# Performance work log

Measured on AMD Instinct MI355X. Metric: run time of the kernel, lower is better.

## Reference

```python
import jax, jax.numpy as jnp
import numpy as np

NUM_HEADS = 16
NUM_LANDMARKS = 64
N_ITER = 6


def iterative_inv(mat):
    # mat: (B, H, L, L) row-stochastic kernel; Newton-Schulz-style iteration
    L = mat.shape[-1]
    I = jnp.eye(L, dtype=mat.dtype)
    K = mat
    # init: V = K^T / max_j(sum_i K_ij)
    denom = jnp.max(jnp.sum(K, axis=-2), axis=-1)[:, :, None, None]
    Vm = (1.0 / denom) * jnp.swapaxes(K, -1, -2)
    for _ in range(N_ITER):
        KV = jnp.matmul(K, Vm)
        Vm = jnp.matmul(0.25 * Vm, 13.0 * I - jnp.matmul(KV, 15.0 * I - jnp.matmul(KV, 7.0 * I - KV)))
    return Vm


def setup_inputs() -> dict:
    key = jax.random.key(0)
    kq, kk, kv = jax.random.split(key, 3)
    B, N, C = 4, 4096, 1024
    return {
        "Q": jax.random.normal(kq, (B, N, C), dtype=jnp.float32),
        "K": jax.random.normal(kk, (B, N, C), dtype=jnp.float32),
        "V": jax.random.normal(kv, (B, N, C), dtype=jnp.float32),
    }


def reference(Q, K, V):
    B, N, C = Q.shape
    H, Lm = NUM_HEADS, NUM_LANDMARKS
    hd = C // H
    scale = hd ** 0.5
    # (B, H, N, hd)
    q = Q.reshape(B, N, H, hd).transpose(0, 2, 1, 3) / scale
    k = K.reshape(B, N, H, hd).transpose(0, 2, 1, 3)
    v = V.reshape(B, N, H, hd).transpose(0, 2, 1, 3)

    # landmark pooling (N divisible by Lm): mean over segments of length N//Lm
    seg = N // Lm
    k_lm = k.reshape(B, H, Lm, seg, hd).mean(axis=-2)  # (B,H,Lm,hd)
    q_lm = q.reshape(B, H, Lm, seg, hd).mean(axis=-2)  # (B,H,Lm,hd)

    kernel_1 = jax.nn.softmax(jnp.einsum('bhnd,bhld->bhnl', q, k_lm), axis=-1)   # (B,H,N,Lm)
    kernel_2 = jax.nn.softmax(jnp.einsum('bhmd,bhld->bhml', q_lm, k_lm), axis=-1)  # (B,H,Lm,Lm)
    kernel_3 = jax.nn.softmax(jnp.einsum('bhld,bhnd->bhln', q_lm, k), axis=-1)   # (B,H,Lm,N)

    out = jnp.matmul(jnp.matmul(kernel_1, iterative_inv(kernel_2)), jnp.matmul(kernel_3, v))
    return out.transpose(0, 2, 1, 3).reshape(B, N, C)
```

## Files before the change

kernel.cpp:

```cpp
#include <hip/hip_runtime.h>
#include <math.h>

#define BB 4
#define NN 4096
#define CC 1024
#define HH 16
#define HD 64
#define LM 64
#define SEG 64
#define BHN (BB*HH)
#define MATP 68
#define MATE (64*MATP)
#define KS 68

typedef __attribute__((ext_vector_type(8))) short bf16x8;
typedef __attribute__((ext_vector_type(4))) short s16x4;
typedef __attribute__((ext_vector_type(4))) float f32x4;

__device__ __forceinline__ float shfl_sum16(float v) {
  v += __shfl_xor(v, 1, 16);
  v += __shfl_xor(v, 2, 16);
  v += __shfl_xor(v, 4, 16);
  v += __shfl_xor(v, 8, 16);
  return v;
}

__device__ __forceinline__ void split8(const float* f, bf16x8& hi, bf16x8& lo) {
#pragma unroll
  for (int i = 0; i < 8; ++i) {
    unsigned u = __builtin_bit_cast(unsigned, f[i]);
    float hf = __builtin_bit_cast(float, u & 0xFFFF0000u);
    hi[i] = (short)(u >> 16);
    float l = f[i] - hf;
    unsigned ul = __builtin_bit_cast(unsigned, l);
    lo[i] = (short)(ul >> 16);
  }
}

__device__ __forceinline__ void split4(const float* f, s16x4& hi, s16x4& lo) {
#pragma unroll
  for (int i = 0; i < 4; ++i) {
    unsigned u = __builtin_bit_cast(unsigned, f[i]);
    float hf = __builtin_bit_cast(float, u & 0xFFFF0000u);
    hi[i] = (short)(u >> 16);
    float l = f[i] - hf;
    unsigned ul = __builtin_bit_cast(unsigned, l);
    lo[i] = (short)(ul >> 16);
  }
}

__device__ __forceinline__ bf16x8 ld8(const short* __restrict__ P, int row, int kb) {
  s16x4 a = *(const s16x4*)&P[row*KS + kb];
  s16x4 b = *(const s16x4*)&P[row*KS + kb + 4];
  bf16x8 r;
  r[0]=a[0]; r[1]=a[1]; r[2]=a[2]; r[3]=a[3];
  r[4]=b[0]; r[5]=b[1]; r[6]=b[2]; r[7]=b[3];
  return r;
}

__device__ __forceinline__ bf16x8 ldT8(const short* __restrict__ P, int row, int kb, int sw) {
  const char* base = (const char*)P + row*136;
  s16x4 a = *(const s16x4*)(base + ((2*kb) ^ sw));
  s16x4 b = *(const s16x4*)(base + ((2*kb + 8) ^ sw));
  bf16x8 r;
  r[0]=a[0]; r[1]=a[1]; r[2]=a[2]; r[3]=a[3];
  r[4]=b[0]; r[5]=b[1]; r[6]=b[2]; r[7]=b[3];
  return r;
}

__device__ __forceinline__ void xpose4(float x[4], int lane) {
  bool p1 = (lane >> 4) & 1;
  float s0 = p1 ? x[0] : x[1], s1 = p1 ? x[2] : x[3];
  float r0 = __shfl_xor(s0, 16, 64), r1 = __shfl_xor(s1, 16, 64);
  if (p1) { x[0] = r0; x[2] = r1; } else { x[1] = r0; x[3] = r1; }
  bool p2 = (lane >> 5) & 1;
  s0 = p2 ? x[0] : x[2]; s1 = p2 ? x[1] : x[3];
  r0 = __shfl_xor(s0, 32, 64); r1 = __shfl_xor(s1, 32, 64);
  if (p2) { x[0] = r0; x[1] = r1; } else { x[2] = r0; x[3] = r1; }
}

__global__ __launch_bounds__(256) void lm_kernel(
    const float* __restrict__ Q, const float* __restrict__ K,
    float* __restrict__ qlm, float* __restrict__ klm) {
  int bh = blockIdx.y; int b = bh >> 4; int h = bh & 15;
  int tid = threadIdx.x;
  int l = blockIdx.x * 4 + (tid >> 6);
  int d = tid & 63;
  const float* qbase = Q + ((size_t)b*NN + (size_t)l*SEG)*CC + h*HD + d;
  const float* kbase = K + ((size_t)b*NN + (size_t)l*SEG)*CC + h*HD + d;
  float sq = 0.f, sk = 0.f;
#pragma unroll 8
  for (int s = 0; s < SEG; ++s) {
    sq += qbase[(size_t)s*CC];
    sk += kbase[(size_t)s*CC];
  }
  qlm[(size_t)bh*4096 + l*64 + d] = sq * (1.0f/(64.0f*8.0f));
  klm[(size_t)bh*4096 + l*64 + d] = sk * (1.0f/64.0f);
}

__global__ __launch_bounds__(256, 3) void k3v_kernel(
    const float* __restrict__ K, const float* __restrict__ V,
    const float* __restrict__ qlm,
    float* __restrict__ S3, float* __restrict__ ACC3) {
  __shared__ short KEh[64*KS], KEl[64*KS];
  __shared__ short VtH[64*KS], VtL[64*KS];
  __shared__ float Erow[64*MATP];
  const int bh = blockIdx.y, b = bh >> 4, h = bh & 15;
  const int tile = blockIdx.x, tid = threadIdx.x;
  const int wid = tid >> 6, lane = tid & 63;
  const int lr = lane & 15, lg = lane >> 4;
  const int m0 = wid*16 + lg*4;

  bf16x8 qh[2], ql[2];
#pragma unroll
  for (int ks = 0; ks < 2; ++ks) {
    const float* qp = qlm + (size_t)bh*4096 + (wid*16 + lr)*64 + ks*32 + lg*8;
    float qf[8];
    *(float4*)&qf[0] = *(const float4*)qp;
    *(float4*)&qf[4] = *(const float4*)(qp + 4);
    split8(qf, qh[ks], ql[ks]);
  }

  f32x4 acc2[4];
#pragma unroll
  for (int t = 0; t < 4; ++t) acc2[t] = (f32x4){0.f, 0.f, 0.f, 0.f};
  float srow[4] = {0.f, 0.f, 0.f, 0.f};

  for (int sub = 0; sub < 4; ++sub) {
    const int n0 = tile*256 + sub*64;
    __syncthreads();
#pragma unroll
    for (int q = 0; q < 4; ++q) {
      int f = tid + 256*q;
      int r = f >> 4, c4 = (f & 15) << 2;
      size_t g = ((size_t)b*NN + n0 + r)*CC + h*HD + c4;
      float4 kv = *(const float4*)&K[g];
      s16x4 kh, kl; split4((const float*)&kv, kh, kl);
      *(s16x4*)&KEh[r*KS + c4] = kh;
      *(s16x4*)&KEl[r*KS + c4] = kl;
      float4 vv = *(const float4*)&V[g];
      float x[4] = {vv.x, vv.y, vv.z, vv.w};
      xpose4(x, lane);
      int d = 4*(lane & 15) + (lane >> 4);
      int nb = 16*q + 4*wid;
      s16x4 vh, vl; split4(x, vh, vl);
      char* pv = (char*)VtH + d*136 + ((2*nb) ^ ((d & 15) << 3));
      char* pl = (char*)VtL + d*136 + ((2*nb) ^ ((d & 15) << 3));
      *(s16x4*)pv = vh;
      *(s16x4*)pl = vl;
    }
    __syncthreads();

    f32x4 zacc[4];
#pragma unroll
    for (int t = 0; t < 4; ++t) zacc[t] = (f32x4){0.f, 0.f, 0.f, 0.f};
#pragma unroll
    for (int ks = 0; ks < 2; ++ks) {
      const int kb = ks*32 + lg*8;
#pragma unroll
      for (int tn = 0; tn < 4; ++tn) {
        bf16x8 bh_ = ld8(KEh, tn*16 + lr, kb);
        bf16x8 bl_ = ld8(KEl, tn*16 + lr, kb);
        zacc[tn] = __builtin_amdgcn_mfma_f32_16x16x32_bf16(qh[ks], bh_, zacc[tn], 0, 0, 0);
        zacc[tn] = __builtin_amdgcn_mfma_f32_16x16x32_bf16(qh[ks], bl_, zacc[tn], 0, 0, 0);
        zacc[tn] = __builtin_amdgcn_mfma_f32_16x16x32_bf16(ql[ks], bh_, zacc[tn], 0, 0, 0);
      }
    }
    float e[4][4];
#pragma unroll
    for (int tn = 0; tn < 4; ++tn)
#pragma unroll
      for (int r = 0; r < 4; ++r) e[tn][r] = expf(zacc[tn][r]);
#pragma unroll
    for (int r = 0; r < 4; ++r) {
      float t = e[0][r] + e[1][r] + e[2][r] + e[3][r];
      srow[r] += shfl_sum16(t);
    }
#pragma unroll
    for (int tn = 0; tn < 4; ++tn) {
      const int n = tn*16 + lr;
#pragma unroll
      for (int r = 0; r < 4; ++r) Erow[(m0 + r)*MATP + n] = e[tn][r];
    }

#pragma unroll
    for (int ks = 0; ks < 2; ++ks) {
      const int kb = ks*32 + lg*8;
      float fa[8];
      const float* ap = Erow + (wid*16 + lr)*MATP + kb;
      *(float4*)&fa[0] = *(const float4*)ap;
      *(float4*)&fa[4] = *(const float4*)(ap + 4);
      bf16x8 ah, al; split8(fa, ah, al);
      const int sw = lr << 3;
#pragma unroll
      for (int tn = 0; tn < 4; ++tn) {
        bf16x8 bh_ = ldT8(VtH, tn*16 + lr, kb, sw);
        bf16x8 bl_ = ldT8(VtL, tn*16 + lr, kb, sw);
        acc2[tn] = __builtin_amdgcn_mfma_f32_16x16x32_bf16(ah, bh_, acc2[tn], 0, 0, 0);
        acc2[tn] = __builtin_amdgcn_mfma_f32_16x16x32_bf16(ah, bl_, acc2[tn], 0, 0, 0);
        acc2[tn] = __builtin_amdgcn_mfma_f32_16x16x32_bf16(al, bh_, acc2[tn], 0, 0, 0);
      }
    }
  }

  if (lr == 0) {
#pragma unroll
    for (int r = 0; r < 4; ++r)
      atomicAdd(&S3[bh*64 + m0 + r], srow[r]);
  }
#pragma unroll
  for (int tn = 0; tn < 4; ++tn)
#pragma unroll
    for (int r = 0; r < 4; ++r)
      atomicAdd(&ACC3[(size_t)bh*4096 + (m0 + r)*64 + tn*16 + lr], acc2[tn][r]);
}

template<bool FUSE, bool HR, bool HC, bool HG>
__device__ __forceinline__ void mm_mfma(
    const float* __restrict__ Arow, const float* __restrict__ Scol,
    float diagc, float scale,
    float* __restrict__ OutRow, float* __restrict__ OutCol, float* __restrict__ OutGlob,
    int wid, int lane) {
  const int lr = lane & 15, lg = lane >> 4;
  f32x4 acc[4];
#pragma unroll
  for (int t = 0; t < 4; ++t) acc[t] = (f32x4){0.f, 0.f, 0.f, 0.f};

#pragma unroll
  for (int ks = 0; ks < 2; ++ks) {
    const int kb = ks*32 + lg*8;
    float fa[8];
    const float* ap = Arow + (wid*16 + lr)*MATP + kb;
#pragma unroll
    for (int i = 0; i < 4; ++i) { float2 t = *(const float2*)(ap + 2*i); fa[2*i] = t.x; fa[2*i+1] = t.y; }
    bf16x8 ah, al; split8(fa, ah, al);
#pragma unroll
    for (int tn = 0; tn < 4; ++tn) {
      float fb[8];
      const float* bp = Scol + (tn*16 + lr)*MATP + kb;
#pragma unroll
      for (int i = 0; i < 4; ++i) { float2 t = *(const float2*)(bp + 2*i); fb[2*i] = t.x; fb[2*i+1] = t.y; }
      if (FUSE) {
        int diff = (tn*16 + lr) - kb;
#pragma unroll
        for (int i = 0; i < 8; ++i) fb[i] = (i == diff ? diagc : 0.f) - fb[i];
      }
      bf16x8 bh_, bl_; split8(fb, bh_, bl_);
      acc[tn] = __builtin_amdgcn_mfma_f32_16x16x32_bf16(ah, bh_, acc[tn], 0, 0, 0);
      acc[tn] = __builtin_amdgcn_mfma_f32_16x16x32_bf16(ah, bl_, acc[tn], 0, 0, 0);
      acc[tn] = __builtin_amdgcn_mfma_f32_16x16x32_bf16(al, bh_, acc[tn], 0, 0, 0);
    }
  }
  __syncthreads();
#pragma unroll
  for (int tn = 0; tn < 4; ++tn) {
    float v0 = scale*acc[tn][0], v1 = scale*acc[tn][1], v2 = scale*acc[tn][2], v3 = scale*acc[tn][3];
    const int n = tn*16 + lr, m0 = wid*16 + lg*4;
    if (HC) *(float4*)&OutCol[n*MATP + m0] = make_float4(v0, v1, v2, v3);
    if (HR) {
      OutRow[(m0+0)*MATP + n] = v0;
      OutRow[(m0+1)*MATP + n] = v1;
      OutRow[(m0+2)*MATP + n] = v2;
      OutRow[(m0+3)*MATP + n] = v3;
    }
    if (HG) {
      OutGlob[(m0+0)*64 + n] = v0;
      OutGlob[(m0+1)*64 + n] = v1;
      OutGlob[(m0+2)*64 + n] = v2;
      OutGlob[(m0+3)*64 + n] = v3;
    }
  }
  __syncthreads();
}

__global__ __launch_bounds__(256) void inv_kernel(
    const float* __restrict__ qlm, const float* __restrict__ klm,
    const float* __restrict__ S3, const float* __restrict__ ACC3,
    float* __restrict__ W) {
  extern __shared__ float sm[];
  float* K2row = sm;
  float* Vmrow = sm + 1*MATE;
  float* Vmcol = sm + 2*MATE;
  float* Xrow  = sm + 3*MATE;
  float* Xcol  = sm + 4*MATE;
  float* Ycol  = sm + 5*MATE;
  float* Zcol  = sm + 6*MATE;
  float* red   = sm + 7*MATE;
  const int bh = blockIdx.x, tid = threadIdx.x;
  const int wid = tid >> 6, lane = tid & 63;
  const int lr = lane & 15, lg = lane >> 4;

#pragma unroll
  for (int q = 0; q < 4; ++q) {
    int f = tid + 256*q;
    int r = f >> 4, c4 = (f & 15) << 2;
    *(float4*)&Xrow[r*MATP + c4] = *(const float4*)&qlm[(size_t)bh*4096 + f*4];
    *(float4*)&Xcol[r*MATP + c4] = *(const float4*)&klm[(size_t)bh*4096 + f*4];
  }
  __syncthreads();

  {
    f32x4 zacc[4];
#pragma unroll
    for (int t = 0; t < 4; ++t) zacc[t] = (f32x4){0.f, 0.f, 0.f, 0.f};
#pragma unroll
    for (int ks = 0; ks < 2; ++ks) {
      const int kb = ks*32 + lg*8;
      float fa[8];
      const float* ap = Xrow + (wid*16 + lr)*MATP + kb;
#pragma unroll
      for (int i = 0; i < 4; ++i) { float2 t = *(const float2*)(ap + 2*i); fa[2*i] = t.x; fa[2*i+1] = t.y; }
      bf16x8 ah, al; split8(fa, ah, al);
#pragma unroll
      for (int tn = 0; tn < 4; ++tn) {
        float fb[8];
        const float* bp = Xcol + (tn*16 + lr)*MATP + kb;
#pragma unroll
        for (int i = 0; i < 4; ++i) { float2 t = *(const float2*)(bp + 2*i); fb[2*i] = t.x; fb[2*i+1] = t.y; }
        bf16x8 bh_, bl_; split8(fb, bh_, bl_);
        zacc[tn] = __builtin_amdgcn_mfma_f32_16x16x32_bf16(ah, bh_, zacc[tn], 0, 0, 0);
        zacc[tn] = __builtin_amdgcn_mfma_f32_16x16x32_bf16(ah, bl_, zacc[tn], 0, 0, 0);
        zacc[tn] = __builtin_amdgcn_mfma_f32_16x16x32_bf16(al, bh_, zacc[tn], 0, 0, 0);
      }
    }
    __syncthreads();
    float e[4][4];
#pragma unroll
    for (int tn = 0; tn < 4; ++tn)
#pragma unroll
      for (int r = 0; r < 4; ++r) e[tn][r] = expf(zacc[tn][r]);
#pragma unroll
    for (int r = 0; r < 4; ++r) {
      float t = e[0][r] + e[1][r] + e[2][r] + e[3][r];
      t = shfl_sum16(t);
      float ri = 1.0f / t;
#pragma unroll
      for (int tn = 0; tn < 4; ++tn) e[tn][r] *= ri;
    }
    const int m0 = wid*16 + lg*4;
#pragma unroll
    for (int tn = 0; tn < 4; ++tn) {
      const int n = tn*16 + lr;
#pragma unroll
      for (int r = 0; r < 4; ++r) K2row[(m0+r)*MATP + n] = e[tn][r];
    }
  }
  __syncthreads();

  if (tid < 64) {
    float c = 0.f;
#pragma unroll 8
    for (int i = 0; i < 64; ++i) c += K2row[i*MATP + tid];
#pragma unroll
    for (int m = 1; m < 64; m <<= 1) c = fmaxf(c, __shfl_xor(c, m, 64));
    if (tid == 0) red[0] = 1.0f / c;
  }
  __syncthreads();
  const float invden = red[0];

#pragma unroll
  for (int q = 0; q < 4; ++q) {
    int f = tid + 256*q;
    int i = f >> 4, c4 = (f & 15) << 2;
    float4 kv = *(const float4*)&K2row[i*MATP + c4];
    kv.x *= invden; kv.y *= invden; kv.z *= invden; kv.w *= invden;
    *(float4*)&Vmcol[i*MATP + c4] = kv;
    Vmrow[(c4+0)*MATP + i] = kv.x;
    Vmrow[(c4+1)*MATP + i] = kv.y;
    Vmrow[(c4+2)*MATP + i] = kv.z;
    Vmrow[(c4+3)*MATP + i] = kv.w;
  }
  __syncthreads();

  for (int it = 0; it < 6; ++it) {
    mm_mfma<false, true,  true,  false>(K2row, Vmcol, 0.f,  1.0f,  Xrow, Xcol, nullptr, wid, lane);
    mm_mfma<true,  false, true,  false>(Xrow,  Xcol,  7.f,  1.0f,  nullptr, Ycol, nullptr, wid, lane);
    mm_mfma<true,  false, true,  false>(Xrow,  Ycol,  15.f, 1.0f,  nullptr, Zcol, nullptr, wid, lane);
    mm_mfma<true,  true,  true,  false>(Vmrow, Zcol,  13.f, 0.25f, Vmrow, Vmcol, nullptr, wid, lane);
  }

#pragma unroll
  for (int q = 0; q < 4; ++q) {
    int f = tid + 256*q;
    int k = f >> 4, c4 = (f & 15) << 2;
    float4 tv = *(const float4*)&ACC3[(size_t)bh*4096 + f*4];
    float ri = 1.0f / S3[bh*64 + k];
    Ycol[(c4+0)*MATP + k] = tv.x * ri;
    Ycol[(c4+1)*MATP + k] = tv.y * ri;
    Ycol[(c4+2)*MATP + k] = tv.z * ri;
    Ycol[(c4+3)*MATP + k] = tv.w * ri;
  }
  __syncthreads();
  mm_mfma<false, false, false, true>(Vmrow, Ycol, 0.f, 1.0f, nullptr, nullptr, W + (size_t)bh*4096, wid, lane);
}

__global__ __launch_bounds__(256, 3) void out_kernel(
    const float* __restrict__ Q, const float* __restrict__ klm,
    const float* __restrict__ W, float* __restrict__ Out) {
  __shared__ short KlH[64*KS], KlL[64*KS];
  __shared__ short WtH[64*KS], WtL[64*KS];
  __shared__ float Prow[64*MATP];
  const int bh = blockIdx.y, b = bh >> 4, h = bh & 15;
  const int n0 = blockIdx.x * 64;
  const int tid = threadIdx.x;
  const int wid = tid >> 6, lane = tid & 63;
  const int lr = lane & 15, lg = lane >> 4;
  const int m0 = wid*16 + lg*4;

#pragma unroll
  for (int q = 0; q < 4; ++q) {
    int f = tid + 256*q;
    int r = f >> 4, c4 = (f & 15) << 2;
    float4 kl = *(const float4*)&klm[(size_t)bh*4096 + f*4];
    s16x4 kh, kll; split4((const float*)&kl, kh, kll);
    *(s16x4*)&KlH[r*KS + c4] = kh;
    *(s16x4*)&KlL[r*KS + c4] = kll;
    float4 wv = *(const float4*)&W[(size_t)bh*4096 + f*4];
    float x[4] = {wv.x, wv.y, wv.z, wv.w};
    xpose4(x, lane);
    int d = 4*(lane & 15) + (lane >> 4);
    int nb = 16*q + 4*wid;
    s16x4 wh, wl; split4(x, wh, wl);
    char* pv = (char*)WtH + d*136 + ((2*nb) ^ ((d & 15) << 3));
    char* pl = (char*)WtL + d*136 + ((2*nb) ^ ((d & 15) << 3));
    *(s16x4*)pv = wh;
    *(s16x4*)pl = wl;
  }

  bf16x8 qh[2], ql[2];
#pragma unroll
  for (int ks = 0; ks < 2; ++ks) {
    const float* qp = Q + ((size_t)b*NN + n0 + wid*16 + lr)*CC + h*HD + ks*32 + lg*8;
    float qf[8];
    *(float4*)&qf[0] = *(const float4*)qp;
    *(float4*)&qf[4] = *(const float4*)(qp + 4);
#pragma unroll
    for (int i = 0; i < 8; ++i) qf[i] *= 0.125f;
    split8(qf, qh[ks], ql[ks]);
  }
  __syncthreads();

  f32x4 zacc[4];
#pragma unroll
  for (int t = 0; t < 4; ++t) zacc[t] = (f32x4){0.f, 0.f, 0.f, 0.f};
#pragma unroll
  for (int ks = 0; ks < 2; ++ks) {
    const int kb = ks*32 + lg*8;
#pragma unroll
    for (int tn = 0; tn < 4; ++tn) {
      bf16x8 bh_ = ld8(KlH, tn*16 + lr, kb);
      bf16x8 bl_ = ld8(KlL, tn*16 + lr, kb);
      zacc[tn] = __builtin_amdgcn_mfma_f32_16x16x32_bf16(qh[ks], bh_, zacc[tn], 0, 0, 0);
      zacc[tn] = __builtin_amdgcn_mfma_f32_16x16x32_bf16(qh[ks], bl_, zacc[tn], 0, 0, 0);
      zacc[tn] = __builtin_amdgcn_mfma_f32_16x16x32_bf16(ql[ks], bh_, zacc[tn], 0, 0, 0);
    }
  }
  float e[4][4];
#pragma unroll
  for (int tn = 0; tn < 4; ++tn)
#pragma unroll
    for (int r = 0; r < 4; ++r) e[tn][r] = expf(zacc[tn][r]);
#pragma unroll
  for (int r = 0; r < 4; ++r) {
    float t = e[0][r] + e[1][r] + e[2][r] + e[3][r];
    t = shfl_sum16(t);
    float ri = 1.0f / t;
#pragma unroll
    for (int tn = 0; tn < 4; ++tn) e[tn][r] *= ri;
  }
#pragma unroll
  for (int tn = 0; tn < 4; ++tn) {
    const int n = tn*16 + lr;
#pragma unroll
    for (int r = 0; r < 4; ++r) Prow[(m0+r)*MATP + n] = e[tn][r];
  }

  f32x4 oacc[4];
#pragma unroll
  for (int t = 0; t < 4; ++t) oacc[t] = (f32x4){0.f, 0.f, 0.f, 0.f};
#pragma unroll
  for (int ks = 0; ks < 2; ++ks) {
    const int kb = ks*32 + lg*8;
    float fa[8];
    const float* ap = Prow + (wid*16 + lr)*MATP + kb;
    *(float4*)&fa[0] = *(const float4*)ap;
    *(float4*)&fa[4] = *(const float4*)(ap + 4);
    bf16x8 ah, al; split8(fa, ah, al);
    const int sw = lr << 3;
#pragma unroll
    for (int tn = 0; tn < 4; ++tn) {
      bf16x8 bh_ = ldT8(WtH, tn*16 + lr, kb, sw);
      bf16x8 bl_ = ldT8(WtL, tn*16 + lr, kb, sw);
      oacc[tn] = __builtin_amdgcn_mfma_f32_16x16x32_bf16(ah, bh_, oacc[tn], 0, 0, 0);
      oacc[tn] = __builtin_amdgcn_mfma_f32_16x16x32_bf16(ah, bl_, oacc[tn], 0, 0, 0);
      oacc[tn] = __builtin_amdgcn_mfma_f32_16x16x32_bf16(al, bh_, oacc[tn], 0, 0, 0);
    }
  }
#pragma unroll
  for (int tn = 0; tn < 4; ++tn) {
    const int d = tn*16 + lr;
#pragma unroll
    for (int r = 0; r < 4; ++r)
      Out[((size_t)b*NN + n0 + m0 + r)*CC + h*HD + d] = oacc[tn][r];
  }
}

extern "C" void kernel_launch(void* const* d_in, const int* in_sizes, int n_in,
                              void* d_out, int out_size, void* d_ws, size_t ws_size,
                              hipStream_t stream) {
  const float* Q = (const float*)d_in[0];
  const float* K = (const float*)d_in[1];
  const float* V = (const float*)d_in[2];
  float* out = (float*)d_out;
  float* ws  = (float*)d_ws;

  float* qlm  = ws;
  float* klm  = ws + 262144;
  float* S3   = ws + 524288;
  float* ACC3 = ws + 528384;
  float* Wm   = ws + 790528;

  size_t shC = (size_t)(7*MATE + 4)*sizeof(float);
  hipFuncSetAttribute((const void*)inv_kernel,
                      hipFuncAttributeMaxDynamicSharedMemorySize, (int)shC);

  hipMemsetAsync(S3, 0, (4096 + 262144)*sizeof(float), stream);

  lm_kernel <<<dim3(16, BHN), 256, 0, stream>>>(Q, K, qlm, klm);
  k3v_kernel<<<dim3(16, BHN), 256, 0, stream>>>(K, V, qlm, S3, ACC3);
  inv_kernel<<<dim3(BHN),     256, shC, stream>>>(qlm, klm, S3, ACC3, Wm);
  out_kernel<<<dim3(64, BHN), 256, 0, stream>>>(Q, klm, Wm, out);
}
```

Measured before the change: 171.7 us.

## Swizzle LDS into dense 128-bit planes, prefetch K/V tiles, double k3v grid

Switches the bf16 hi/lo LDS tiles to an unpadded 128-byte-row layout with an XOR swizzle, so B-operand fragments load as single 128-bit reads instead of two 64-bit reads. The k3v kernel now handles 128 rows per block on a grid twice as large, and loads the next tile's K/V from global memory into registers while computing the current tile. expf is replaced by __expf in the softmax paths. The changes add register pressure and more atomic adds into the shared accumulators, and slightly reduce exp accuracy.

```diff
diff --git a/kernel.cpp b/kernel.cpp
--- a/kernel.cpp
+++ b/kernel.cpp
@@ -11,7 +11,6 @@
 #define BHN (BB*HH)
 #define MATP 68
 #define MATE (64*MATP)
-#define KS 68
 
 typedef __attribute__((ext_vector_type(8))) short bf16x8;
 typedef __attribute__((ext_vector_type(4))) short s16x4;
@@ -49,23 +48,12 @@
   }
 }
 
-__device__ __forceinline__ bf16x8 ld8(const short* __restrict__ P, int row, int kb) {
-  s16x4 a = *(const s16x4*)&P[row*KS + kb];
-  s16x4 b = *(const s16x4*)&P[row*KS + kb + 4];
-  bf16x8 r;
-  r[0]=a[0]; r[1]=a[1]; r[2]=a[2]; r[3]=a[3];
-  r[4]=b[0]; r[5]=b[1]; r[6]=b[2]; r[7]=b[3];
-  return r;
-}
-
-__device__ __forceinline__ bf16x8 ldT8(const short* __restrict__ P, int row, int kb, int sw) {
-  const char* base = (const char*)P + row*136;
-  s16x4 a = *(const s16x4*)(base + ((2*kb) ^ sw));
-  s16x4 b = *(const s16x4*)(base + ((2*kb + 8) ^ sw));
-  bf16x8 r;
-  r[0]=a[0]; r[1]=a[1]; r[2]=a[2]; r[3]=a[3];
-  r[4]=b[0]; r[5]=b[1]; r[6]=b[2]; r[7]=b[3];
-  return r;
+__device__ __forceinline__ int planeAddr(int row, int cd) {
+  int B = (row << 7) + (cd << 4);
+  return B ^ ((row & 7) << 4);
+}
+__device__ __forceinline__ bf16x8 ldP(const short* __restrict__ P, int row, int cd) {
+  return *(const bf16x8*)((const char*)P + planeAddr(row, cd));
 }
 
 __device__ __forceinline__ void xpose4(float x[4], int lane) {
@@ -102,9 +90,9 @@
     const float* __restrict__ K, const float* __restrict__ V,
     const float* __restrict__ qlm,
     float* __restrict__ S3, float* __restrict__ ACC3) {
-  __shared__ short KEh[64*KS], KEl[64*KS];
-  __shared__ short VtH[64*KS], VtL[64*KS];
-  __shared__ float Erow[64*MATP];
+  __shared__ alignas(16) short KEh[64*64], KEl[64*64];
+  __shared__ alignas(16) short VtH[64*64], VtL[64*64];
+  __shared__ alignas(16) float Erow[64*MATP];
   const int bh = blockIdx.y, b = bh >> 4, h = bh & 15;
   const int tile = blockIdx.x, tid = threadIdx.x;
   const int wid = tid >> 6, lane = tid & 63;
@@ -126,82 +114,112 @@
   for (int t = 0; t < 4; ++t) acc2[t] = (f32x4){0.f, 0.f, 0.f, 0.f};
   float srow[4] = {0.f, 0.f, 0.f, 0.f};
 
-  for (int sub = 0; sub < 4; ++sub) {
-    const int n0 = tile*256 + sub*64;
-    __syncthreads();
-#pragma unroll
-    for (int q = 0; q < 4; ++q) {
-      int f = tid + 256*q;
-      int r = f >> 4, c4 = (f & 15) << 2;
-      size_t g = ((size_t)b*NN + n0 + r)*CC + h*HD + c4;
-      float4 kv = *(const float4*)&K[g];
-      s16x4 kh, kl; split4((const float*)&kv, kh, kl);
-      *(s16x4*)&KEh[r*KS + c4] = kh;
-      *(s16x4*)&KEl[r*KS + c4] = kl;
-      float4 vv = *(const float4*)&V[g];
-      float x[4] = {vv.x, vv.y, vv.z, vv.w};
-      xpose4(x, lane);
-      int d = 4*(lane & 15) + (lane >> 4);
-      int nb = 16*q + 4*wid;
-      s16x4 vh, vl; split4(x, vh, vl);
-      char* pv = (char*)VtH + d*136 + ((2*nb) ^ ((d & 15) << 3));
-      char* pl = (char*)VtL + d*136 + ((2*nb) ^ ((d & 15) << 3));
-      *(s16x4*)pv = vh;
-      *(s16x4*)pl = vl;
-    }
-    __syncthreads();
-
-    f32x4 zacc[4];
-#pragma unroll
-    for (int t = 0; t < 4; ++t) zacc[t] = (f32x4){0.f, 0.f, 0.f, 0.f};
-#pragma unroll
-    for (int ks = 0; ks < 2; ++ks) {
-      const int kb = ks*32 + lg*8;
-#pragma unroll
-      for (int tn = 0; tn < 4; ++tn) {
-        bf16x8 bh_ = ld8(KEh, tn*16 + lr, kb);
-        bf16x8 bl_ = ld8(KEl, tn*16 + lr, kb);
-        zacc[tn] = __builtin_amdgcn_mfma_f32_16x16x32_bf16(qh[ks], bh_, zacc[tn], 0, 0, 0);
-        zacc[tn] = __builtin_amdgcn_mfma_f32_16x16x32_bf16(qh[ks], bl_, zacc[tn], 0, 0, 0);
-        zacc[tn] = __builtin_amdgcn_mfma_f32_16x16x32_bf16(ql[ks], bh_, zacc[tn], 0, 0, 0);
-      }
-    }
-    float e[4][4];
-#pragma unroll
-    for (int tn = 0; tn < 4; ++tn)
-#pragma unroll
-      for (int r = 0; r < 4; ++r) e[tn][r] = expf(zacc[tn][r]);
-#pragma unroll
-    for (int r = 0; r < 4; ++r) {
-      float t = e[0][r] + e[1][r] + e[2][r] + e[3][r];
-      srow[r] += shfl_sum16(t);
-    }
-#pragma unroll
-    for (int tn = 0; tn < 4; ++tn) {
-      const int n = tn*16 + lr;
-#pragma unroll
-      for (int r = 0; r < 4; ++r) Erow[(m0 + r)*MATP + n] = e[tn][r];
-    }
-
-#pragma unroll
-    for (int ks = 0; ks < 2; ++ks) {
-      const int kb = ks*32 + lg*8;
-      float fa[8];
-      const float* ap = Erow + (wid*16 + lr)*MATP + kb;
-      *(float4*)&fa[0] = *(const float4*)ap;
-      *(float4*)&fa[4] = *(const float4*)(ap + 4);
-      bf16x8 ah, al; split8(fa, ah, al);
-      const int sw = lr << 3;
-#pragma unroll
-      for (int tn = 0; tn < 4; ++tn) {
-        bf16x8 bh_ = ldT8(VtH, tn*16 + lr, kb, sw);
-        bf16x8 bl_ = ldT8(VtL, tn*16 + lr, kb, sw);
-        acc2[tn] = __builtin_amdgcn_mfma_f32_16x16x32_bf16(ah, bh_, acc2[tn], 0, 0, 0);
-        acc2[tn] = __builtin_amdgcn_mfma_f32_16x16x32_bf16(ah, bl_, acc2[tn], 0, 0, 0);
-        acc2[tn] = __builtin_amdgcn_mfma_f32_16x16x32_bf16(al, bh_, acc2[tn], 0, 0, 0);
-      }
-    }
-  }
+  const int rk0 = tid >> 3,        ck = tid & 7;
+  const int rk1 = (tid + 256) >> 3;
+  const int dV  = 4*lr + lg;
+
+  float4 gk[2][2], gv[4];
+
+#define K3V_LOAD(SUB)                                                          \
+  {                                                                            \
+    const int n0_ = tile*128 + (SUB)*64;                                       \
+    const float* kb0 = &K[((size_t)b*NN + n0_ + rk0)*CC + h*HD + ck*8];        \
+    const float* kb1 = &K[((size_t)b*NN + n0_ + rk1)*CC + h*HD + ck*8];        \
+    gk[0][0] = *(const float4*)kb0;  gk[0][1] = *(const float4*)(kb0 + 4);     \
+    gk[1][0] = *(const float4*)kb1;  gk[1][1] = *(const float4*)(kb1 + 4);     \
+    _Pragma("unroll")                                                          \
+    for (int q = 0; q < 4; ++q) {                                              \
+      int f = tid + 256*q;                                                     \
+      int r = f >> 4, c4 = (f & 15) << 2;                                      \
+      gv[q] = *(const float4*)&V[((size_t)b*NN + n0_ + r)*CC + h*HD + c4];     \
+    }                                                                          \
+  }
+
+#define K3V_WRITE()                                                            \
+  {                                                                            \
+    _Pragma("unroll")                                                          \
+    for (int q2 = 0; q2 < 2; ++q2) {                                           \
+      float kf[8];                                                             \
+      *(float4*)&kf[0] = gk[q2][0];                                            \
+      *(float4*)&kf[4] = gk[q2][1];                                            \
+      bf16x8 khv, klv; split8(kf, khv, klv);                                   \
+      int r = q2 ? rk1 : rk0;                                                  \
+      int A = planeAddr(r, ck);                                                \
+      *(bf16x8*)((char*)KEh + A) = khv;                                        \
+      *(bf16x8*)((char*)KEl + A) = klv;                                        \
+    }                                                                          \
+    _Pragma("unroll")                                                          \
+    for (int q = 0; q < 4; ++q) {                                              \
+      float x[4] = {gv[q].x, gv[q].y, gv[q].z, gv[q].w};                       \
+      xpose4(x, lane);                                                         \
+      int nb = 16*q + 4*wid;                                                   \
+      s16x4 vh, vl; split4(x, vh, vl);                                         \
+      int B = (dV << 7) + (nb << 1);                                           \
+      B ^= (dV & 7) << 4;                                                      \
+      *(s16x4*)((char*)VtH + B) = vh;                                          \
+      *(s16x4*)((char*)VtL + B) = vl;                                          \
+    }                                                                          \
+  }
+
+#define K3V_COMPUTE()                                                          \
+  {                                                                            \
+    f32x4 zacc[4];                                                             \
+    _Pragma("unroll")                                                          \
+    for (int t = 0; t < 4; ++t) zacc[t] = (f32x4){0.f, 0.f, 0.f, 0.f};        \
+    _Pragma("unroll")                                                          \
+    for (int ks = 0; ks < 2; ++ks) {                                           \
+      _Pragma("unroll")                                                        \
+      for (int tn = 0; tn < 4; ++tn) {                                         \
+        bf16x8 bh_ = ldP(KEh, tn*16 + lr, 4*ks + lg);                          \
+        bf16x8 bl_ = ldP(KEl, tn*16 + lr, 4*ks + lg);                          \
+        zacc[tn] = __builtin_amdgcn_mfma_f32_16x16x32_bf16(qh[ks], bh_, zacc[tn], 0, 0, 0); \
+        zacc[tn] = __builtin_amdgcn_mfma_f32_16x16x32_bf16(qh[ks], bl_, zacc[tn], 0, 0, 0); \
+        zacc[tn] = __builtin_amdgcn_mfma_f32_16x16x32_bf16(ql[ks], bh_, zacc[tn], 0, 0, 0); \
+      }                                                                        \
+    }                                                                          \
+    float e[4][4];                                                             \
+    _Pragma("unroll")                                                          \
+    for (int tn = 0; tn < 4; ++tn)                                             \
+      _Pragma("unroll")                                                        \
+      for (int r = 0; r < 4; ++r) e[tn][r] = __expf(zacc[tn][r]);              \
+    _Pragma("unroll")                                                          \
+    for (int r = 0; r < 4; ++r) {                                              \
+      float t = e[0][r] + e[1][r] + e[2][r] + e[3][r];                         \
+      srow[r] += shfl_sum16(t);                                                \
+    }                                                                          \
+    _Pragma("unroll")                                                          \
+    for (int tn = 0; tn < 4; ++tn) {                                           \
+      const int n = tn*16 + lr;                                                \
+      _Pragma("unroll")                                                        \
+      for (int r = 0; r < 4; ++r) Erow[(m0 + r)*MATP + n] = e[tn][r];          \
+    }                                                                          \
+    _Pragma("unroll")                                                          \
+    for (int ks = 0; ks < 2; ++ks) {                                           \
+      float fa[8];                                                             \
+      const float* ap = Erow + (wid*16 + lr)*MATP + ks*32 + lg*8;              \
+      *(float4*)&fa[0] = *(const float4*)ap;                                   \
+      *(float4*)&fa[4] = *(const float4*)(ap + 4);                             \
+      bf16x8 ah, al; split8(fa, ah, al);                                       \
+      _Pragma("unroll")                                                        \
+      for (int tn = 0; tn < 4; ++tn) {                                         \
+        bf16x8 bh_ = ldP(VtH, tn*16 + lr, 4*ks + lg);                          \
+        bf16x8 bl_ = ldP(VtL, tn*16 + lr, 4*ks + lg);                          \
+        acc2[tn] = __builtin_amdgcn_mfma_f32_16x16x32_bf16(ah, bh_, acc2[tn], 0, 0, 0); \
+        acc2[tn] = __builtin_amdgcn_mfma_f32_16x16x32_bf16(ah, bl_, acc2[tn], 0, 0, 0); \
+        acc2[tn] = __builtin_amdgcn_mfma_f32_16x16x32_bf16(al, bh_, acc2[tn], 0, 0, 0); \
+      }                                                                        \
+    }                                                                          \
+  }
+
+  K3V_LOAD(0)
+  K3V_WRITE()
+  __syncthreads();
+  K3V_LOAD(1)
+  K3V_COMPUTE()
+  __syncthreads();
+  K3V_WRITE()
+  __syncthreads();
+  K3V_COMPUTE()
 
   if (lr == 0) {
 #pragma unroll
@@ -328,7 +346,7 @@
 #pragma unroll
     for (int tn = 0; tn < 4; ++tn)
 #pragma unroll
-      for (int r = 0; r < 4; ++r) e[tn][r] = expf(zacc[tn][r]);
+      for (int r = 0; r < 4; ++r) e[tn][r] = __expf(zacc[tn][r]);
 #pragma unroll
     for (int r = 0; r < 4; ++r) {
       float t = e[0][r] + e[1][r] + e[2][r] + e[3][r];
@@ -397,9 +415,9 @@
 __global__ __launch_bounds__(256, 3) void out_kernel(
     const float* __restrict__ Q, const float* __restrict__ klm,
     const float* __restrict__ W, float* __restrict__ Out) {
-  __shared__ short KlH[64*KS], KlL[64*KS];
-  __shared__ short WtH[64*KS], WtL[64*KS];
-  __shared__ float Prow[64*MATP];
+  __shared__ alignas(16) short KlH[64*64], KlL[64*64];
+  __shared__ alignas(16) short WtH[64*64], WtL[64*64];
+  __shared__ alignas(16) float Prow[64*MATP];
   const int bh = blockIdx.y, b = bh >> 4, h = bh & 15;
   const int n0 = blockIdx.x * 64;
   const int tid = threadIdx.x;
@@ -408,26 +426,35 @@
   const int m0 = wid*16 + lg*4;
 
 #pragma unroll
+  for (int q2 = 0; q2 < 2; ++q2) {
+    int f = tid + 256*q2;
+    int r = f >> 3, c = f & 7;
+    const float* kp = &klm[(size_t)bh*4096 + r*64 + c*8];
+    float kf[8];
+    *(float4*)&kf[0] = *(const float4*)kp;
+    *(float4*)&kf[4] = *(const float4*)(kp + 4);
+    bf16x8 khv, klv; split8(kf, khv, klv);
+    int A = planeAddr(r, c);
+    *(bf16x8*)((char*)KlH + A) = khv;
+    *(bf16x8*)((char*)KlL + A) = klv;
+  }
+  const int dW = 4*lr + lg;
+#pragma unroll
   for (int q = 0; q < 4; ++q) {
     int f = tid + 256*q;
     int r = f >> 4, c4 = (f & 15) << 2;
-    float4 kl = *(const float4*)&klm[(size_t)bh*4096 + f*4];
-    s16x4 kh, kll; split4((const float*)&kl, kh, kll);
-    *(s16x4*)&KlH[r*KS + c4] = kh;
-    *(s16x4*)&KlL[r*KS + c4] = kll;
-    float4 wv = *(const float4*)&W[(size_t)bh*4096 + f*4];
+    float4 wv = *(const float4*)&W[(size_t)bh*4096 + r*64 + c4];
     float x[4] = {wv.x, wv.y, wv.z, wv.w};
     xpose4(x, lane);
-    int d = 4*(lane & 15) + (lane >> 4);
     int nb = 16*q + 4*wid;
     s16x4 wh, wl; split4(x, wh, wl);
-    char* pv = (char*)WtH + d*136 + ((2*nb) ^ ((d & 15) << 3));
-    char* pl = (char*)WtL + d*136 + ((2*nb) ^ ((d & 15) << 3));
-    *(s16x4*)pv = wh;
-    *(s16x4*)pl = wl;
-  }
-
-  bf16x8 qh[2], ql[2];
+    int B = (dW << 7) + (nb << 1);
+    B ^= (dW & 7) << 4;
+    *(s16x4*)((char*)WtH + B) = wh;
+    *(s16x4*)((char*)WtL + B) = wl;
+  }
+
+  bf16x8 qh[2], qlo[2];
 #pragma unroll
   for (int ks = 0; ks < 2; ++ks) {
     const float* qp = Q + ((size_t)b*NN + n0 + wid*16 + lr)*CC + h*HD + ks*32 + lg*8;
@@ -436,7 +463,7 @@
     *(float4*)&qf[4] = *(const float4*)(qp + 4);
 #pragma unroll
     for (int i = 0; i < 8; ++i) qf[i] *= 0.125f;
-    split8(qf, qh[ks], ql[ks]);
+    split8(qf, qh[ks], qlo[ks]);
   }
   __syncthreads();
 
@@ -445,21 +472,20 @@
   for (int t = 0; t < 4; ++t) zacc[t] = (f32x4){0.f, 0.f, 0.f, 0.f};
 #pragma unroll
   for (int ks = 0; ks < 2; ++ks) {
-    const int kb = ks*32 + lg*8;
 #pragma unroll
     for (int tn = 0; tn < 4; ++tn) {
-      bf16x8 bh_ = ld8(KlH, tn*16 + lr, kb);
-      bf16x8 bl_ = ld8(KlL, tn*16 + lr, kb);
+      bf16x8 bh_ = ldP(KlH, tn*16 + lr, 4*ks + lg);
+      bf16x8 bl_ = ldP(KlL, tn*16 + lr, 4*ks + lg);
       zacc[tn] = __builtin_amdgcn_mfma_f32_16x16x32_bf16(qh[ks], bh_, zacc[tn], 0, 0, 0);
       zacc[tn] = __builtin_amdgcn_mfma_f32_16x16x32_bf16(qh[ks], bl_, zacc[tn], 0, 0, 0);
-      zacc[tn] = __builtin_amdgcn_mfma_f32_16x16x32_bf16(ql[ks], bh_, zacc[tn], 0, 0, 0);
+      zacc[tn] = __builtin_amdgcn_mfma_f32_16x16x32_bf16(qlo[ks], bh_, zacc[tn], 0, 0, 0);
     }
   }
   float e[4][4];
 #pragma unroll
   for (int tn = 0; tn < 4; ++tn)
 #pragma unroll
-    for (int r = 0; r < 4; ++r) e[tn][r] = expf(zacc[tn][r]);
+    for (int r = 0; r < 4; ++r) e[tn][r] = __expf(zacc[tn][r]);
 #pragma unroll
   for (int r = 0; r < 4; ++r) {
     float t = e[0][r] + e[1][r] + e[2][r] + e[3][r];
@@ -480,17 +506,15 @@
   for (int t = 0; t < 4; ++t) oacc[t] = (f32x4){0.f, 0.f, 0.f, 0.f};
 #pragma unroll
   for (int ks = 0; ks < 2; ++ks) {
-    const int kb = ks*32 + lg*8;
     float fa[8];
-    const float* ap = Prow + (wid*16 + lr)*MATP + kb;
+    const float* ap = Prow + (wid*16 + lr)*MATP + ks*32 + lg*8;
     *(float4*)&fa[0] = *(const float4*)ap;
     *(float4*)&fa[4] = *(const float4*)(ap + 4);
     bf16x8 ah, al; split8(fa, ah, al);
-    const int sw = lr << 3;
 #pragma unroll
     for (int tn = 0; tn < 4; ++tn) {
-      bf16x8 bh_ = ldT8(WtH, tn*16 + lr, kb, sw);
-      bf16x8 bl_ = ldT8(WtL, tn*16 + lr, kb, sw);
+      bf16x8 bh_ = ldP(WtH, tn*16 + lr, 4*ks + lg);
+      bf16x8 bl_ = ldP(WtL, tn*16 + lr, 4*ks + lg);
       oacc[tn] = __builtin_amdgcn_mfma_f32_16x16x32_bf16(ah, bh_, oacc[tn], 0, 0, 0);
       oacc[tn] = __builtin_amdgcn_mfma_f32_16x16x32_bf16(ah, bl_, oacc[tn], 0, 0, 0);
       oacc[tn] = __builtin_amdgcn_mfma_f32_16x16x32_bf16(al, bh_, oacc[tn], 0, 0, 0);
@@ -527,7 +551,7 @@
   hipMemsetAsync(S3, 0, (4096 + 262144)*sizeof(float), stream);
 
   lm_kernel <<<dim3(16, BHN), 256, 0, stream>>>(Q, K, qlm, klm);
-  k3v_kernel<<<dim3(16, BHN), 256, 0, stream>>>(K, V, qlm, S3, ACC3);
+  k3v_kernel<<<dim3(32, BHN), 256, 0, stream>>>(K, V, qlm, S3, ACC3);
   inv_kernel<<<dim3(BHN),     256, shC, stream>>>(qlm, klm, S3, ACC3, Wm);
   out_kernel<<<dim3(64, BHN), 256, 0, stream>>>(Q, klm, Wm, out);
 }
```

Measured after the change: 147.7 us. -14.0%, faster.
